# Kernel tuning notes

Hardware: AMD Instinct MI355X
Metric: run time of the kernel (lower is better)

Reference implementation:

```python
import jax, jax.numpy as jnp
import numpy as np

N_TREES = 64
DEPTH = 10           # complete binary trees
ARITY = 2
C = 8                # hidden states
M = 32               # observation labels
G = 8                # n_gen
NPT = 2 ** (DEPTH + 1) - 1   # nodes per tree = 2047
DIM = N_TREES * NPT          # 131008 total nodes


def _levels(parents_cat, children_cat):
    # Static (Python-int) slicing: level d has N_TREES * 2**d children.
    levels, pos = [], 0
    for d in range(1, DEPTH + 1):
        n = N_TREES * (2 ** d)
        levels.append((parents_cat[pos:pos + n], children_cat[pos:pos + n]))
        pos += n
    return levels


def _forward(A, B, Pi, x, roots, leaves, inv_map, trees_ind, parents_cat, children_cat):
    sm_A = jax.nn.softmax(A, axis=0)    # (C,C,G), columns sum to 1 over first axis
    sm_B = jax.nn.softmax(B, axis=1)    # (C,M,G)
    sm_Pi = jax.nn.softmax(Pi, axis=0)  # (C,G)
    log_A, log_Pi = jnp.log(sm_A), jnp.log(sm_Pi)

    levels = _levels(parents_cat, children_cat)
    obs = x[inv_map]
    emit = lambda idx: jnp.transpose(sm_B[:, obs[idx]], (1, 0, 2))  # (n,C,G)

    # ---- preliminary downward: prior[n,i,g] ----
    prior = jnp.zeros((DIM, C, G), dtype=A.dtype)
    prior = prior.at[roots].set(jnp.broadcast_to(sm_Pi, (roots.shape[0], C, G)))
    for pa, ch in levels:
        prior = prior.at[ch].set(jnp.einsum('ijg,njg->nig', sm_A, prior[pa]))

    # ---- upward (beta recursion) ----
    beta = jnp.zeros((DIM, C, G), dtype=A.dtype)
    t_beta = jnp.zeros((DIM, C, G), dtype=A.dtype)
    bl = prior[leaves] * emit(leaves)
    beta = beta.at[leaves].set(bl / bl.sum(1, keepdims=True))
    for pa, ch in reversed(levels):
        ratio = beta[ch] / prior[ch]                       # (n,C,G)
        beta_uv = jnp.einsum('ijg,nig->njg', sm_A, ratio)  # message child->parent
        t_beta = t_beta.at[ch].set(beta_uv)
        u_idx = pa[::ARITY]                                # unique parents (children are contiguous pairs)
        prod_u = beta_uv.reshape(-1, ARITY, C, G).prod(axis=1)  # segmented product over siblings
        bu = prior[u_idx] * emit(u_idx) * prod_u
        beta = beta.at[u_idx].set(bu / bu.sum(1, keepdims=True))

    # ---- downward (eps / t_eps posteriors) ----
    eps = jnp.zeros((DIM, C, G), dtype=A.dtype)
    t_eps = jnp.zeros((DIM, C, C, G), dtype=A.dtype)
    eps = eps.at[roots].set(beta[roots])
    for pa, ch in levels:
        pa_factor = eps[pa][:, None, :, :] * sm_A[None] / t_beta[ch][:, None, :, :]  # (n,C,C,G)
        ch_factor = (beta[ch] / prior[ch])[:, :, None, :]                            # (n,C,1,G)
        te = ch_factor * pa_factor
        t_eps = t_eps.at[ch].set(te)
        num = te.sum(2)
        eps = eps.at[ch].set(num / num.sum(1, keepdims=True))

    # ---- log likelihood, scattered per tree ----
    lik = jnp.zeros((DIM, G), dtype=A.dtype)
    lik = lik.at[roots].add((eps[roots] * log_Pi[None]).sum(1))
    no_root = jnp.concatenate([ch for _, ch in levels])
    lik = lik.at[no_root].add((t_eps[no_root] * log_A[None]).sum((1, 2)))
    internal = jnp.concatenate([pa[::ARITY] for pa, _ in levels])
    all_nodes = jnp.concatenate([internal, leaves])
    lik = lik.at[all_nodes].add((eps[all_nodes] * jnp.log(emit(all_nodes))).sum(1))
    ll = jax.ops.segment_sum(lik, trees_ind, num_segments=N_TREES)  # (N_TREES, G)
    return -ll


def setup_inputs() -> dict:
    key = jax.random.key(0)
    kA, kB, kPi, kx = jax.random.split(key, 4)
    A = jax.random.normal(kA, (C, C, G), dtype=jnp.float32)
    B = jax.random.normal(kB, (C, M, G), dtype=jnp.float32)
    Pi = jax.random.normal(kPi, (C, G), dtype=jnp.float32)
    x = jax.random.randint(kx, (DIM,), 0, M, dtype=jnp.int32)

    offsets = np.arange(N_TREES, dtype=np.int64) * NPT
    parents, children = [], []
    for d in range(1, DEPTH + 1):
        cl = np.arange(2 ** d - 1, 2 ** (d + 1) - 1)   # local child indices at level d
        pl = (cl - 1) // 2                             # local parent indices
        children.append((offsets[:, None] + cl[None, :]).ravel())
        parents.append((offsets[:, None] + pl[None, :]).ravel())
    parents_cat = jnp.asarray(np.concatenate(parents), dtype=jnp.int32)
    children_cat = jnp.asarray(np.concatenate(children), dtype=jnp.int32)
    leaves = jnp.asarray(children[-1], dtype=jnp.int32)
    roots = jnp.asarray(offsets, dtype=jnp.int32)
    inv_map = jnp.arange(DIM, dtype=jnp.int32)
    trees_ind = jnp.asarray(np.repeat(np.arange(N_TREES), NPT), dtype=jnp.int32)
    return {"A": A, "B": B, "Pi": Pi, "x": x, "roots": roots, "leaves": leaves,
            "inv_map": inv_map, "trees_ind": trees_ind,
            "parents_cat": parents_cat, "children_cat": children_cat}


def reference(A, B, Pi, x, roots, leaves, inv_map, trees_ind, parents_cat, children_cat):
    return _forward(A, B, Pi, x, roots, leaves, inv_map, trees_ind, parents_cat, children_cat)
```

## Files before the change

kernel.cpp:

```cpp
#include <hip/hip_runtime.h>


#define NTREES 64
#define DEPTH  10
#define C      8
#define M      32
#define G      8
#define NPT    2047
#define PAD    9
#define BLOCK  256

__global__ __launch_bounds__(BLOCK, 2)
void htmm_kernel(const float* __restrict__ A,
                 const float* __restrict__ B,
                 const float* __restrict__ Pi,
                 const int*   __restrict__ x,
                 float* __restrict__ out)
{
    __shared__ float buf[NPT * PAD];
    __shared__ float sA[C][C],  lgA[C][C];
    __shared__ float sB[C][M],  lgB[C][M];
    __shared__ float spi[C],    lgpi[C];
    __shared__ float red[BLOCK];

    const int b   = blockIdx.x;
    const int t   = b >> 3;
    const int g   = b & 7;
    const int tid = threadIdx.x;
    const int nodeBase = t * NPT;

    if (tid < C) {
        const int j = tid;
        float v[C]; float mx = -1e30f;
        for (int i = 0; i < C; ++i) { v[i] = A[(i*C + j)*G + g]; mx = fmaxf(mx, v[i]); }
        float s = 0.f;
        for (int i = 0; i < C; ++i) { v[i] = expf(v[i] - mx); s += v[i]; }
        const float inv = 1.f / s;
        for (int i = 0; i < C; ++i) { const float sm = v[i]*inv; sA[i][j] = sm; lgA[i][j] = logf(sm); }
    } else if (tid >= 64 && tid < 64 + C) {
        const int c = tid - 64;
        float v[M]; float mx = -1e30f;
        for (int m = 0; m < M; ++m) { v[m] = B[(c*M + m)*G + g]; mx = fmaxf(mx, v[m]); }
        float s = 0.f;
        for (int m = 0; m < M; ++m) { v[m] = expf(v[m] - mx); s += v[m]; }
        const float inv = 1.f / s;
        for (int m = 0; m < M; ++m) { const float sm = v[m]*inv; sB[c][m] = sm; lgB[c][m] = logf(sm); }
    } else if (tid == 128) {
        float v[C]; float mx = -1e30f;
        for (int c = 0; c < C; ++c) { v[c] = Pi[c*G + g]; mx = fmaxf(mx, v[c]); }
        float s = 0.f;
        for (int c = 0; c < C; ++c) { v[c] = expf(v[c] - mx); s += v[c]; }
        const float inv = 1.f / s;
        for (int c = 0; c < C; ++c) { const float sm = v[c]*inv; spi[c] = sm; lgpi[c] = logf(sm); }
    }
    __syncthreads();

    if (tid == 0) {
        for (int i = 0; i < C; ++i) buf[i] = spi[i];
    }
    __syncthreads();
    for (int d = 1; d <= DEPTH; ++d) {
        const int start = (1 << d) - 1, cnt = 1 << d;
        for (int v = start + tid; v < start + cnt; v += BLOCK) {
            const int pa = (v - 1) >> 1;
            float p[C];
            #pragma unroll
            for (int j = 0; j < C; ++j) p[j] = buf[pa*PAD + j];
            #pragma unroll
            for (int i = 0; i < C; ++i) {
                float acc = 0.f;
                #pragma unroll
                for (int j = 0; j < C; ++j) acc += sA[i][j] * p[j];
                buf[v*PAD + i] = acc;
            }
        }
        __syncthreads();
    }

    {
        const int start = (1 << DEPTH) - 1, cnt = 1 << DEPTH;
        for (int v = start + tid; v < start + cnt; v += BLOCK) {
            const int xv = x[nodeBase + v];
            float e[C]; float Z = 0.f;
            #pragma unroll
            for (int i = 0; i < C; ++i) { e[i] = sB[i][xv]; Z += buf[v*PAD + i] * e[i]; }
            const float invZ = 1.f / Z;
            #pragma unroll
            for (int i = 0; i < C; ++i) buf[v*PAD + i] = e[i] * invZ;
        }
        __syncthreads();
    }
    for (int d = DEPTH - 1; d >= 0; --d) {
        const int start = (1 << d) - 1, cnt = 1 << d;
        for (int u = start + tid; u < start + cnt; u += BLOCK) {
            const int c1 = 2*u + 1, c2 = 2*u + 2;
            float r1[C], r2[C];
            #pragma unroll
            for (int i = 0; i < C; ++i) { r1[i] = buf[c1*PAD + i]; r2[i] = buf[c2*PAD + i]; }
            float prod[C];
            #pragma unroll
            for (int j = 0; j < C; ++j) {
                float a1 = 0.f, a2 = 0.f;
                #pragma unroll
                for (int i = 0; i < C; ++i) { a1 += sA[i][j]*r1[i]; a2 += sA[i][j]*r2[i]; }
                prod[j] = a1 * a2;
            }
            const int xu = x[nodeBase + u];
            float pr[C], ep[C]; float Z = 0.f;
            #pragma unroll
            for (int j = 0; j < C; ++j) {
                ep[j] = sB[j][xu] * prod[j];
                pr[j] = buf[u*PAD + j];
                Z += pr[j] * ep[j];
            }
            const float invZ = 1.f / Z;
            if (u == 0) {
                #pragma unroll
                for (int j = 0; j < C; ++j) buf[j] = pr[j] * ep[j] * invZ;
            } else {
                #pragma unroll
                for (int j = 0; j < C; ++j) buf[u*PAD + j] = ep[j] * invZ;
            }
        }
        __syncthreads();
    }

    float lik = 0.f;
    if (tid == 0) {
        const int xr = x[nodeBase];
        #pragma unroll
        for (int c = 0; c < C; ++c) lik += buf[c] * (lgpi[c] + lgB[c][xr]);
    }
    for (int d = 1; d <= DEPTH; ++d) {
        const int start = (1 << d) - 1, cnt = 1 << d;
        for (int v = start + tid; v < start + cnt; v += BLOCK) {
            const int pa = (v - 1) >> 1;
            float epa[C], r[C];
            #pragma unroll
            for (int j = 0; j < C; ++j) epa[j] = buf[pa*PAD + j];
            #pragma unroll
            for (int i = 0; i < C; ++i) r[i] = buf[v*PAD + i];
            float f[C];
            #pragma unroll
            for (int j = 0; j < C; ++j) {
                float tb = 0.f;
                #pragma unroll
                for (int i = 0; i < C; ++i) tb += sA[i][j] * r[i];
                f[j] = epa[j] / tb;
            }
            float num[C], S = 0.f, likA = 0.f;
            #pragma unroll
            for (int i = 0; i < C; ++i) {
                float a = 0.f, la = 0.f;
                #pragma unroll
                for (int j = 0; j < C; ++j) {
                    const float te = sA[i][j] * f[j];
                    a  += te;
                    la += te * lgA[i][j];
                }
                num[i] = r[i] * a;
                S     += num[i];
                likA  += r[i] * la;
            }
            const int xv = x[nodeBase + v];
            const float invS = 1.f / S;
            float likE = 0.f;
            #pragma unroll
            for (int i = 0; i < C; ++i) {
                const float e2 = num[i] * invS;
                buf[v*PAD + i] = e2;
                likE += e2 * lgB[i][xv];
            }
            lik += likA + likE;
        }
        __syncthreads();
    }

    red[tid] = lik;
    __syncthreads();
    for (int off = BLOCK >> 1; off > 0; off >>= 1) {
        if (tid < off) red[tid] += red[tid + off];
        __syncthreads();
    }
    if (tid == 0) out[t*G + g] = -red[0];
}

extern "C" void kernel_launch(void* const* d_in, const int* in_sizes, int n_in,
                              void* d_out, int out_size, void* d_ws, size_t ws_size,
                              hipStream_t stream) {
    const float* A  = (const float*)d_in[0];
    const float* B  = (const float*)d_in[1];
    const float* Pi = (const float*)d_in[2];
    const int*   x  = (const int*)d_in[3];
    float* out = (float*)d_out;
    htmm_kernel<<<NTREES * G, BLOCK, 0, stream>>>(A, B, Pi, x, out);
}
```

Baseline: 115.8 us.

## Keep bottom two tree levels in registers and shrink shared buffer

Each of 512 threads now owns one level-9 node and its two leaf children, holding their priors, betas and posteriors in registers. Only the top 1023 nodes live in shared memory. This cuts LDS footprint, removes two barrier-separated levels, and fuses the leaf work into the per-thread pass. It also precomputes A*logA so the log is never taken per node, uses a hardware reciprocal, writes sibling priors once per parent, and reduces with wave shuffles. The fast reciprocal slightly loosens precision, and more registers per thread could limit occupancy.

Result: slower. 120.7 us (+4.3%).

```diff
diff --git a/kernel.cpp b/kernel.cpp
--- a/kernel.cpp
+++ b/kernel.cpp
@@ -8,181 +8,249 @@
 #define G      8
 #define NPT    2047
 #define PAD    9
-#define BLOCK  256
-
-__global__ __launch_bounds__(BLOCK, 2)
+#define BLOCK  512
+#define LNODES 1023
+
+__device__ __forceinline__ float frcp(float v) { return __builtin_amdgcn_rcpf(v); }
+
+__global__ __launch_bounds__(BLOCK, 4)
 void htmm_kernel(const float* __restrict__ A,
                  const float* __restrict__ B,
                  const float* __restrict__ Pi,
                  const int*   __restrict__ x,
                  float* __restrict__ out)
 {
-    __shared__ float buf[NPT * PAD];
-    __shared__ float sA[C][C],  lgA[C][C];
-    __shared__ float sB[C][M],  lgB[C][M];
-    __shared__ float spi[C],    lgpi[C];
-    __shared__ float red[BLOCK];
+    __shared__ float buf[LNODES * PAD];
+    __shared__ float sA[C][C], sAL[C][C];
+    __shared__ float sB[C][M], lgB[C][M];
+    __shared__ float spi[C],  lgpi[C];
+    __shared__ float bls[C];
+    __shared__ float red8[BLOCK / 64];
 
     const int b   = blockIdx.x;
     const int t   = b >> 3;
     const int g   = b & 7;
     const int tid = threadIdx.x;
-    const int nodeBase = t * NPT;
+    const int base = t * NPT;
 
     if (tid < C) {
         const int j = tid;
-        float v[C]; float mx = -1e30f;
-        for (int i = 0; i < C; ++i) { v[i] = A[(i*C + j)*G + g]; mx = fmaxf(mx, v[i]); }
-        float s = 0.f;
-        for (int i = 0; i < C; ++i) { v[i] = expf(v[i] - mx); s += v[i]; }
-        const float inv = 1.f / s;
-        for (int i = 0; i < C; ++i) { const float sm = v[i]*inv; sA[i][j] = sm; lgA[i][j] = logf(sm); }
+        float w[C]; float mx = -1e30f;
+        #pragma unroll
+        for (int i = 0; i < C; ++i) { w[i] = A[(i*C + j)*G + g]; mx = fmaxf(mx, w[i]); }
+        float s = 0.f; float e[C];
+        #pragma unroll
+        for (int i = 0; i < C; ++i) { e[i] = expf(w[i] - mx); s += e[i]; }
+        const float inv = 1.f / s, ls = logf(s);
+        #pragma unroll
+        for (int i = 0; i < C; ++i) {
+            const float sm = e[i] * inv;
+            sA[i][j]  = sm;
+            sAL[i][j] = sm * ((w[i] - mx) - ls);
+        }
+    } else if (tid == 8) {
+        float w[C]; float mx = -1e30f;
+        #pragma unroll
+        for (int c = 0; c < C; ++c) { w[c] = Pi[c*G + g]; mx = fmaxf(mx, w[c]); }
+        float s = 0.f; float e[C];
+        #pragma unroll
+        for (int c = 0; c < C; ++c) { e[c] = expf(w[c] - mx); s += e[c]; }
+        const float inv = 1.f / s, ls = logf(s);
+        #pragma unroll
+        for (int c = 0; c < C; ++c) { spi[c] = e[c]*inv; lgpi[c] = (w[c]-mx) - ls; }
     } else if (tid >= 64 && tid < 64 + C) {
         const int c = tid - 64;
-        float v[M]; float mx = -1e30f;
-        for (int m = 0; m < M; ++m) { v[m] = B[(c*M + m)*G + g]; mx = fmaxf(mx, v[m]); }
+        float mx = -1e30f;
+        for (int m = 0; m < M; ++m) mx = fmaxf(mx, B[(c*M + m)*G + g]);
         float s = 0.f;
-        for (int m = 0; m < M; ++m) { v[m] = expf(v[m] - mx); s += v[m]; }
-        const float inv = 1.f / s;
-        for (int m = 0; m < M; ++m) { const float sm = v[m]*inv; sB[c][m] = sm; lgB[c][m] = logf(sm); }
-    } else if (tid == 128) {
-        float v[C]; float mx = -1e30f;
-        for (int c = 0; c < C; ++c) { v[c] = Pi[c*G + g]; mx = fmaxf(mx, v[c]); }
-        float s = 0.f;
-        for (int c = 0; c < C; ++c) { v[c] = expf(v[c] - mx); s += v[c]; }
-        const float inv = 1.f / s;
-        for (int c = 0; c < C; ++c) { const float sm = v[c]*inv; spi[c] = sm; lgpi[c] = logf(sm); }
-    }
-    __syncthreads();
-
-    if (tid == 0) {
+        for (int m = 0; m < M; ++m) s += expf(B[(c*M + m)*G + g] - mx);
+        bls[c] = mx + logf(s);
+    }
+    __syncthreads();
+
+    if (tid < C * M) {
+        const int c = tid >> 5, m = tid & 31;
+        const float d0 = B[(c*M + m)*G + g] - bls[c];
+        lgB[c][m] = d0;
+        sB[c][m]  = expf(d0);
+    }
+    if (tid == 320) {
+        #pragma unroll
         for (int i = 0; i < C; ++i) buf[i] = spi[i];
     }
     __syncthreads();
-    for (int d = 1; d <= DEPTH; ++d) {
-        const int start = (1 << d) - 1, cnt = 1 << d;
-        for (int v = start + tid; v < start + cnt; v += BLOCK) {
-            const int pa = (v - 1) >> 1;
+
+    for (int d = 1; d <= 8; ++d) {
+        const int half = 1 << (d - 1);
+        if (tid < half) {
+            const int u = half - 1 + tid;
+            const int cb = 2*u + 1;
             float p[C];
             #pragma unroll
-            for (int j = 0; j < C; ++j) p[j] = buf[pa*PAD + j];
+            for (int j = 0; j < C; ++j) p[j] = buf[u*PAD + j];
             #pragma unroll
             for (int i = 0; i < C; ++i) {
                 float acc = 0.f;
                 #pragma unroll
                 for (int j = 0; j < C; ++j) acc += sA[i][j] * p[j];
-                buf[v*PAD + i] = acc;
+                buf[cb*PAD + i]       = acc;
+                buf[(cb + 1)*PAD + i] = acc;
             }
         }
         __syncthreads();
     }
 
+    const int s  = 511 + tid;
+    const int xs = x[base + s];
+    const int x1 = x[base + 2*s + 1];
+    const int x2 = x[base + 2*s + 2];
+
+    float ps[C], pc[C];
     {
-        const int start = (1 << DEPTH) - 1, cnt = 1 << DEPTH;
-        for (int v = start + tid; v < start + cnt; v += BLOCK) {
-            const int xv = x[nodeBase + v];
-            float e[C]; float Z = 0.f;
-            #pragma unroll
-            for (int i = 0; i < C; ++i) { e[i] = sB[i][xv]; Z += buf[v*PAD + i] * e[i]; }
-            const float invZ = 1.f / Z;
-            #pragma unroll
-            for (int i = 0; i < C; ++i) buf[v*PAD + i] = e[i] * invZ;
-        }
-        __syncthreads();
-    }
-    for (int d = DEPTH - 1; d >= 0; --d) {
-        const int start = (1 << d) - 1, cnt = 1 << d;
-        for (int u = start + tid; u < start + cnt; u += BLOCK) {
-            const int c1 = 2*u + 1, c2 = 2*u + 2;
-            float r1[C], r2[C];
-            #pragma unroll
-            for (int i = 0; i < C; ++i) { r1[i] = buf[c1*PAD + i]; r2[i] = buf[c2*PAD + i]; }
-            float prod[C];
+        const int pas = 255 + (tid >> 1);
+        float pp[C];
+        #pragma unroll
+        for (int j = 0; j < C; ++j) pp[j] = buf[pas*PAD + j];
+        #pragma unroll
+        for (int i = 0; i < C; ++i) {
+            float a = 0.f;
+            #pragma unroll
+            for (int j = 0; j < C; ++j) a += sA[i][j] * pp[j];
+            ps[i] = a;
+        }
+        #pragma unroll
+        for (int i = 0; i < C; ++i) {
+            float a = 0.f;
+            #pragma unroll
+            for (int j = 0; j < C; ++j) a += sA[i][j] * ps[j];
+            pc[i] = a;
+        }
+    }
+
+    float rs[C], r1[C], r2[C];
+    {
+        float e1[C], e2[C]; float Z1 = 0.f, Z2 = 0.f;
+        #pragma unroll
+        for (int i = 0; i < C; ++i) {
+            e1[i] = sB[i][x1]; Z1 += pc[i] * e1[i];
+            e2[i] = sB[i][x2]; Z2 += pc[i] * e2[i];
+        }
+        const float i1 = frcp(Z1), i2 = frcp(Z2);
+        #pragma unroll
+        for (int i = 0; i < C; ++i) { r1[i] = e1[i]*i1; r2[i] = e2[i]*i2; }
+        float Z = 0.f, ep[C];
+        #pragma unroll
+        for (int j = 0; j < C; ++j) {
+            float a1 = 0.f, a2 = 0.f;
+            #pragma unroll
+            for (int i = 0; i < C; ++i) { a1 += sA[i][j]*r1[i]; a2 += sA[i][j]*r2[i]; }
+            ep[j] = sB[j][xs] * (a1 * a2);
+            Z += ps[j] * ep[j];
+        }
+        const float iz = frcp(Z);
+        #pragma unroll
+        for (int j = 0; j < C; ++j) { rs[j] = ep[j]*iz; buf[s*PAD + j] = rs[j]; }
+    }
+    __syncthreads();
+
+    for (int d = 8; d >= 0; --d) {
+        if (tid < (1 << d)) {
+            const int u = (1 << d) - 1 + tid;
+            const int c1 = 2*u + 1;
+            float rr1[C], rr2[C];
+            #pragma unroll
+            for (int i = 0; i < C; ++i) { rr1[i] = buf[c1*PAD + i]; rr2[i] = buf[(c1+1)*PAD + i]; }
+            const int xu = x[base + u];
+            float pr[C], ep[C]; float Z = 0.f;
             #pragma unroll
             for (int j = 0; j < C; ++j) {
                 float a1 = 0.f, a2 = 0.f;
                 #pragma unroll
-                for (int i = 0; i < C; ++i) { a1 += sA[i][j]*r1[i]; a2 += sA[i][j]*r2[i]; }
-                prod[j] = a1 * a2;
-            }
-            const int xu = x[nodeBase + u];
-            float pr[C], ep[C]; float Z = 0.f;
-            #pragma unroll
-            for (int j = 0; j < C; ++j) {
-                ep[j] = sB[j][xu] * prod[j];
+                for (int i = 0; i < C; ++i) { a1 += sA[i][j]*rr1[i]; a2 += sA[i][j]*rr2[i]; }
+                ep[j] = sB[j][xu] * (a1 * a2);
                 pr[j] = buf[u*PAD + j];
                 Z += pr[j] * ep[j];
             }
-            const float invZ = 1.f / Z;
-            if (u == 0) {
-                #pragma unroll
-                for (int j = 0; j < C; ++j) buf[j] = pr[j] * ep[j] * invZ;
+            const float iz = frcp(Z);
+            if (d) {
+                #pragma unroll
+                for (int j = 0; j < C; ++j) buf[u*PAD + j] = ep[j]*iz;
             } else {
                 #pragma unroll
-                for (int j = 0; j < C; ++j) buf[u*PAD + j] = ep[j] * invZ;
+                for (int j = 0; j < C; ++j) buf[j] = pr[j]*ep[j]*iz;
             }
         }
         __syncthreads();
     }
+
+    auto child_node = [&](const float* r, const float* epa, int xv, float* eout) -> float {
+        float f[C];
+        #pragma unroll
+        for (int j = 0; j < C; ++j) {
+            float tb = 0.f;
+            #pragma unroll
+            for (int i = 0; i < C; ++i) tb += sA[i][j] * r[i];
+            f[j] = epa[j] * frcp(tb);
+        }
+        float S = 0.f, likA = 0.f, num[C];
+        #pragma unroll
+        for (int i = 0; i < C; ++i) {
+            float a = 0.f, la = 0.f;
+            #pragma unroll
+            for (int j = 0; j < C; ++j) { a += sA[i][j]*f[j]; la += sAL[i][j]*f[j]; }
+            num[i] = r[i]*a; S += num[i]; likA += r[i]*la;
+        }
+        const float invS = frcp(S);
+        float likE = 0.f;
+        #pragma unroll
+        for (int i = 0; i < C; ++i) {
+            const float e2 = num[i]*invS;
+            if (eout) eout[i] = e2;
+            likE += e2 * lgB[i][xv];
+        }
+        return likA + likE;
+    };
 
     float lik = 0.f;
     if (tid == 0) {
-        const int xr = x[nodeBase];
+        const int xr = x[base];
         #pragma unroll
         for (int c = 0; c < C; ++c) lik += buf[c] * (lgpi[c] + lgB[c][xr]);
     }
-    for (int d = 1; d <= DEPTH; ++d) {
-        const int start = (1 << d) - 1, cnt = 1 << d;
-        for (int v = start + tid; v < start + cnt; v += BLOCK) {
-            const int pa = (v - 1) >> 1;
-            float epa[C], r[C];
+    for (int d = 1; d <= 8; ++d) {
+        if (tid < (1 << d)) {
+            const int v = (1 << d) - 1 + tid, pa = (v - 1) >> 1;
+            float epa[C], r[C], eo[C];
             #pragma unroll
             for (int j = 0; j < C; ++j) epa[j] = buf[pa*PAD + j];
             #pragma unroll
             for (int i = 0; i < C; ++i) r[i] = buf[v*PAD + i];
-            float f[C];
-            #pragma unroll
-            for (int j = 0; j < C; ++j) {
-                float tb = 0.f;
-                #pragma unroll
-                for (int i = 0; i < C; ++i) tb += sA[i][j] * r[i];
-                f[j] = epa[j] / tb;
-            }
-            float num[C], S = 0.f, likA = 0.f;
-            #pragma unroll
-            for (int i = 0; i < C; ++i) {
-                float a = 0.f, la = 0.f;
-                #pragma unroll
-                for (int j = 0; j < C; ++j) {
-                    const float te = sA[i][j] * f[j];
-                    a  += te;
-                    la += te * lgA[i][j];
-                }
-                num[i] = r[i] * a;
-                S     += num[i];
-                likA  += r[i] * la;
-            }
-            const int xv = x[nodeBase + v];
-            const float invS = 1.f / S;
-            float likE = 0.f;
-            #pragma unroll
-            for (int i = 0; i < C; ++i) {
-                const float e2 = num[i] * invS;
-                buf[v*PAD + i] = e2;
-                likE += e2 * lgB[i][xv];
-            }
-            lik += likA + likE;
+            lik += child_node(r, epa, x[base + v], eo);
+            #pragma unroll
+            for (int i = 0; i < C; ++i) buf[v*PAD + i] = eo[i];
         }
         __syncthreads();
     }
-
-    red[tid] = lik;
-    __syncthreads();
-    for (int off = BLOCK >> 1; off > 0; off >>= 1) {
-        if (tid < off) red[tid] += red[tid + off];
-        __syncthreads();
-    }
-    if (tid == 0) out[t*G + g] = -red[0];
+    {
+        const int pas = 255 + (tid >> 1);
+        float epa[C], es[C];
+        #pragma unroll
+        for (int j = 0; j < C; ++j) epa[j] = buf[pas*PAD + j];
+        lik += child_node(rs, epa, xs, es);
+        lik += child_node(r1, es, x1, nullptr);
+        lik += child_node(r2, es, x2, nullptr);
+    }
+
+    #pragma unroll
+    for (int off = 32; off; off >>= 1) lik += __shfl_xor(lik, off, 64);
+    if ((tid & 63) == 0) red8[tid >> 6] = lik;
+    __syncthreads();
+    if (tid == 0) {
+        float acc = 0.f;
+        #pragma unroll
+        for (int w = 0; w < BLOCK/64; ++w) acc += red8[w];
+        out[t*G + g] = -acc;
+    }
 }
 
 extern "C" void kernel_launch(void* const* d_in, const int* in_sizes, int n_in,
```
